# Optimization experiments

Measured on AMD Instinct MI355X. Metric: run time of the kernel, lower is better.

Reference implementation:

```python
import jax, jax.numpy as jnp
import numpy as np

LAM = 0.43
IN_DIM = 256
BATCH = 512


def _persistence_pairs(D):
    """0-dim persistence pairs via Kruskal-style union-find (matches torch code).
    D: [n, n] numpy distance matrix. Returns [n-1, 2] int array of MST edges."""
    n = D.shape[0]
    parent = np.arange(n)

    def find(u):
        root = u
        while parent[root] != root:
            root = parent[root]
        while parent[u] != root:  # path compression
            parent[u], u = root, parent[u]
        return root

    iu, ju = np.triu_indices(n)  # includes diagonal, like triu_indices_from
    w = D[iu, ju]
    order = np.argsort(w, kind='stable')
    pairs = []
    for e in order:
        u, v = int(iu[e]), int(ju[e])
        ru, rv = find(u), find(v)
        if ru == rv:
            continue
        if ru > rv:
            parent[rv] = ru  # merge(v, u)
        else:
            parent[ru] = rv  # merge(u, v)
        pairs.append((u, v) if u < v else (v, u))
    return np.asarray(pairs, dtype=np.int64)  # exactly n-1 edges


def _pdist(x):
    # torch.norm(x[:, None] - x, dim=2, p=2)
    return jnp.linalg.norm(x[:, None, :] - x[None, :, :], axis=-1)


def setup_inputs() -> dict:
    key = jax.random.key(0)
    ks = jax.random.split(key, 16)
    d = IN_DIM
    dims = [(d, d // 2), (d // 2, d // 4), (d // 4, 2), (2, d // 4), (d // 4, d // 2), (d // 2, d)]
    inp = {
        'x': jax.random.normal(ks[0], (BATCH, d), dtype=jnp.float32),
        'label': jax.random.randint(ks[1], (BATCH,), 0, 10),
    }
    names = ['1', '2', 'm', '3', '4', '5']
    for i, (nm, (din, dout)) in enumerate(zip(names, dims)):
        s = 1.0 / np.sqrt(din)
        inp['W' + nm] = jax.random.uniform(ks[2 + 2 * i], (din, dout), minval=-s, maxval=s, dtype=jnp.float32)
        inp['b' + nm] = jax.random.uniform(ks[3 + 2 * i], (dout,), minval=-s, maxval=s, dtype=jnp.float32)
    inp['latent_norm'] = jnp.ones((1,), dtype=jnp.float32)
    return inp


def reference(x, label, W1, b1, W2, b2, Wm, bm, W3, b3, W4, b4, W5, b5, latent_norm):
    # Encoder
    h1 = jax.nn.relu(x @ W1 + b1)
    h2 = jax.nn.relu(h1 @ W2 + b2)
    lat = h2 @ Wm + bm  # [B, 2]

    # normalized pairwise distance matrices
    xd = _pdist(x)
    xd = xd / xd.max()  # 2D-input branch
    ld = _pdist(lat) / latent_norm[0]

    # Decoder
    h3 = jax.nn.relu(lat @ W3 + b3)
    h4 = jax.nn.relu(h3 @ W4 + b4)
    xr = h4 @ W5 + b5
    ae_loss = jnp.mean((x - xr) ** 2)

    # persistence pairs (detached / host computation, as in the torch code)
    p1 = _persistence_pairs(np.asarray(jax.device_get(xd)))
    p2 = _persistence_pairs(np.asarray(jax.device_get(ld)))

    sig1 = xd[p1[:, 0], p1[:, 1]]
    sig1_2 = ld[p1[:, 0], p1[:, 1]]
    sig2 = ld[p2[:, 0], p2[:, 1]]
    sig2_1 = xd[p2[:, 0], p2[:, 1]]
    topo = jnp.sum((sig1 - sig1_2) ** 2) + jnp.sum((sig2 - sig2_1) ** 2)

    loss = ae_loss + LAM * topo / float(x.shape[0])
    return loss
```

## Files before the change

### kernel.cpp

```cpp
#include <hip/hip_runtime.h>
#include <math.h>

#define N      512
#define DIN    256
#define LAM    0.43f
#define MAGIC  0x4D535431u
#define PAD(j) ((j) + (((j) >> 6) << 2))

#define OFF_LDREADY 4
#define OFF_T0READY 5
#define OFF_T0BITS  6
#define OFF_BLKMAX  8
#define OFF_AEPART  128
#define OFF_LAT     1024
#define OFF_XD      2048
#define OFF_LD      (2048 + 262144)
#define OFF_CAND    526336
#define OFF_BAR     (OFF_CAND + 18432)

__device__ __forceinline__ unsigned ld_acq(unsigned* p) {
    return __hip_atomic_load(p, __ATOMIC_ACQUIRE, __HIP_MEMORY_SCOPE_AGENT);
}
__device__ __forceinline__ void st_rel(unsigned* p, unsigned v) {
    __hip_atomic_store(p, v, __ATOMIC_RELEASE, __HIP_MEMORY_SCOPE_AGENT);
}
__device__ __forceinline__ unsigned ld_rlx(unsigned* p) {
    return __hip_atomic_load(p, __ATOMIC_RELAXED, __HIP_MEMORY_SCOPE_AGENT);
}
__device__ __forceinline__ unsigned long long ld64_rlx(unsigned long long* p) {
    return __hip_atomic_load(p, __ATOMIC_RELAXED, __HIP_MEMORY_SCOPE_AGENT);
}
__device__ __forceinline__ void st64_rlx(unsigned long long* p, unsigned long long v) {
    __hip_atomic_store(p, v, __ATOMIC_RELAXED, __HIP_MEMORY_SCOPE_AGENT);
}
__device__ __forceinline__ void spin_magic(unsigned* p) {
    while (ld_acq(p) != MAGIC) __builtin_amdgcn_s_sleep(1);
}

__global__ __launch_bounds__(256) void fused_mlp_pdistx_kernel(
    const float* __restrict__ x,
    const float* __restrict__ W1, const float* __restrict__ b1,
    const float* __restrict__ W2, const float* __restrict__ b2,
    const float* __restrict__ Wm, const float* __restrict__ bm,
    const float* __restrict__ W3, const float* __restrict__ b3,
    const float* __restrict__ W4, const float* __restrict__ b4,
    const float* __restrict__ W5, const float* __restrict__ b5,
    float* __restrict__ lat_out, float* __restrict__ ae_part,
    float* __restrict__ xd, float* __restrict__ blkmax)
{
    const int tid = threadIdx.x;

    if (blockIdx.x < 512) {
        __shared__ float xs[256];
        __shared__ float h1[128];
        __shared__ float h2[64];
        __shared__ float latv[2];
        __shared__ float h3[64];
        __shared__ float h4[128];
        __shared__ float red[4];

        const int row = blockIdx.x;
        xs[tid] = x[(size_t)row * DIN + tid];
        __syncthreads();

        if (tid < 128) {
            float s = b1[tid];
            for (int k = 0; k < 256; ++k) s = fmaf(xs[k], W1[k * 128 + tid], s);
            h1[tid] = fmaxf(s, 0.f);
        }
        __syncthreads();

        if (tid < 64) {
            float s = b2[tid];
            for (int k = 0; k < 128; ++k) s = fmaf(h1[k], W2[k * 64 + tid], s);
            h2[tid] = fmaxf(s, 0.f);
        }
        __syncthreads();

        if (tid < 2) {
            float s = bm[tid];
            for (int k = 0; k < 64; ++k) s = fmaf(h2[k], Wm[k * 2 + tid], s);
            latv[tid] = s;
            lat_out[(size_t)row * 2 + tid] = s;
        }
        __syncthreads();

        if (tid < 64) {
            float s = b3[tid];
            s = fmaf(latv[0], W3[tid], s);
            s = fmaf(latv[1], W3[64 + tid], s);
            h3[tid] = fmaxf(s, 0.f);
        }
        __syncthreads();

        if (tid < 128) {
            float s = b4[tid];
            for (int k = 0; k < 64; ++k) s = fmaf(h3[k], W4[k * 128 + tid], s);
            h4[tid] = fmaxf(s, 0.f);
        }
        __syncthreads();

        float s = b5[tid];
        for (int k = 0; k < 128; ++k) s = fmaf(h4[k], W5[k * 256 + tid], s);
        float diff = xs[tid] - s;
        float a = diff * diff;

        #pragma unroll
        for (int m = 1; m < 64; m <<= 1) a += __shfl_xor(a, m, 64);
        if ((tid & 63) == 0) red[tid >> 6] = a;
        __syncthreads();
        if (tid == 0) ae_part[row] = red[0] + red[1] + red[2] + red[3];
    } else {
        __shared__ float As[32][65];
        __shared__ float Bs[32][65];
        __shared__ float red2[4];

        const int bid = blockIdx.x - 512;
        const int bi = bid & 7, bj = bid >> 3;
        const int i0 = bi * 64, j0 = bj * 64;
        const int ty = tid >> 4, tx = tid & 15;

        float acc[4][4];
        #pragma unroll
        for (int i = 0; i < 4; ++i)
            #pragma unroll
            for (int j = 0; j < 4; ++j) acc[i][j] = 0.f;

        for (int kk = 0; kk < DIN; kk += 32) {
            #pragma unroll
            for (int s = tid; s < 512; s += 256) {
                int r = s >> 3, c4 = (s & 7) << 2;
                float4 va = *(const float4*)(x + (size_t)(i0 + r) * DIN + kk + c4);
                As[c4 + 0][r] = va.x; As[c4 + 1][r] = va.y;
                As[c4 + 2][r] = va.z; As[c4 + 3][r] = va.w;
                float4 vb = *(const float4*)(x + (size_t)(j0 + r) * DIN + kk + c4);
                Bs[c4 + 0][r] = vb.x; Bs[c4 + 1][r] = vb.y;
                Bs[c4 + 2][r] = vb.z; Bs[c4 + 3][r] = vb.w;
            }
            __syncthreads();
            #pragma unroll 8
            for (int k = 0; k < 32; ++k) {
                float a[4], b[4];
                #pragma unroll
                for (int i = 0; i < 4; ++i) a[i] = As[k][ty + 16 * i];
                #pragma unroll
                for (int j = 0; j < 4; ++j) b[j] = Bs[k][tx + 16 * j];
                #pragma unroll
                for (int i = 0; i < 4; ++i)
                    #pragma unroll
                    for (int j = 0; j < 4; ++j) {
                        float d = a[i] - b[j];
                        acc[i][j] = fmaf(d, d, acc[i][j]);
                    }
            }
            __syncthreads();
        }

        float lmax = 0.f;
        #pragma unroll
        for (int i = 0; i < 4; ++i)
            #pragma unroll
            for (int j = 0; j < 4; ++j) {
                float dd = sqrtf(acc[i][j]);
                int r = i0 + ty + 16 * i, c = j0 + tx + 16 * j;
                xd[(size_t)r * N + c] = dd;
                lmax = fmaxf(lmax, dd);
            }

        #pragma unroll
        for (int m = 32; m >= 1; m >>= 1) lmax = fmaxf(lmax, __shfl_xor(lmax, m, 64));
        if ((tid & 63) == 0) red2[tid >> 6] = lmax;
        __syncthreads();
        if (tid == 0)
            blkmax[bid] = fmaxf(fmaxf(red2[0], red2[1]), fmaxf(red2[2], red2[3]));
    }
}

__global__ __launch_bounds__(256) void mst_boruvka_kernel(
    const float* __restrict__ xd, float* __restrict__ ld,
    const float* __restrict__ lat, const float* __restrict__ latent_norm,
    const float* __restrict__ blkmax, const float* __restrict__ ae_part,
    float* __restrict__ wsf, float* __restrict__ out)
{
    __shared__ unsigned comp_a[512];
    __shared__ __align__(16) unsigned comp_s[544];
    __shared__ unsigned long long cval[512];
    __shared__ int tgt[512];
    __shared__ unsigned short eu[512], ev[512];
    __shared__ float ew[512];
    __shared__ float latx[512], laty[512];
    __shared__ float s_red[4];
    __shared__ float s_xdm;
    __shared__ int s_ecnt;

    const int tid = threadIdx.x;
    const int blk = blockIdx.x;
    const int m   = blk >> 6;
    const int wb  = blk & 63;
    const bool leader = (wb == 0);

    unsigned* ldready = (unsigned*)(wsf + OFF_LDREADY);
    unsigned* t0ready = (unsigned*)(wsf + OFF_T0READY);
    unsigned* t0bits  = (unsigned*)(wsf + OFF_T0BITS);
    unsigned long long* candm =
        (unsigned long long*)(wsf + OFF_CAND) + (size_t)m * 9 * 512;
    unsigned* bar = (unsigned*)(wsf + OFF_BAR) + (size_t)m * 640;

    const float* Dm = m ? ld : xd;
    const float* Om = m ? xd : ld;

    if (m == 1) {
        for (int i = tid; i < 512; i += 256) {
            latx[i] = lat[2 * i + 0];
            laty[i] = lat[2 * i + 1];
        }
        __syncthreads();
        const int r0 = wb << 3;
        for (int q = tid; q < 1024; q += 256) {
            int rr = r0 + (q >> 7);
            int j  = (q & 127) << 2;
            float xi = latx[rr], yi = laty[rr];
            float dx0 = xi - latx[j + 0], dy0 = yi - laty[j + 0];
            float dx1 = xi - latx[j + 1], dy1 = yi - laty[j + 1];
            float dx2 = xi - latx[j + 2], dy2 = yi - laty[j + 2];
            float dx3 = xi - latx[j + 3], dy3 = yi - laty[j + 3];
            float4 o;
            o.x = sqrtf(fmaf(dx0, dx0, dy0 * dy0));
            o.y = sqrtf(fmaf(dx1, dx1, dy1 * dy1));
            o.z = sqrtf(fmaf(dx2, dx2, dy2 * dy2));
            o.w = sqrtf(fmaf(dx3, dx3, dy3 * dy3));
            *(float4*)(ld + (size_t)rr * N + j) = o;
        }
    }

    for (int i = tid; i < 72; i += 256)
        st64_rlx(&candm[(size_t)wb * 72 + i], ~0ULL);

    for (int i = tid; i < 512; i += 256) {
        comp_a[i] = (unsigned)i;
        comp_s[PAD(i)] = (unsigned)i;
    }
    if (tid == 0) s_ecnt = 0;

    __syncthreads();
    if (tid == 0) st_rel(&bar[wb], MAGIC);
    if (tid < 64) spin_magic(&bar[tid]);
    __syncthreads();
    if (m == 1 && leader && tid == 0) st_rel(ldready, MAGIC);

    int nc = 512;
    for (int p = 0; p < 9 && nc > 1; ++p) {
        unsigned long long* cand = candm + (size_t)p * 512;

        {
            const int r  = (wb << 3) + (tid >> 5);
            const int c0 = (tid & 31) << 4;
            const unsigned cv = comp_s[PAD(r)];
            const float4* rp = (const float4*)(Dm + (size_t)r * N + c0);
            unsigned long long bk = ~0ULL;
            #pragma unroll
            for (int c = 0; c < 4; ++c) {
                float4 f = rp[c];
                int jb = c0 + 4 * c;
                int4 cc = *(const int4*)&comp_s[PAD(jb)];
                unsigned long long k;
                k = ((unsigned long long)__float_as_uint(f.x) << 18)
                  | ((unsigned long long)r << 9) | (unsigned)(jb + 0);
                if ((unsigned)cc.x != cv && k < bk) bk = k;
                k = ((unsigned long long)__float_as_uint(f.y) << 18)
                  | ((unsigned long long)r << 9) | (unsigned)(jb + 1);
                if ((unsigned)cc.y != cv && k < bk) bk = k;
                k = ((unsigned long long)__float_as_uint(f.z) << 18)
                  | ((unsigned long long)r << 9) | (unsigned)(jb + 2);
                if ((unsigned)cc.z != cv && k < bk) bk = k;
                k = ((unsigned long long)__float_as_uint(f.w) << 18)
                  | ((unsigned long long)r << 9) | (unsigned)(jb + 3);
                if ((unsigned)cc.w != cv && k < bk) bk = k;
            }
            #pragma unroll
            for (int mm = 1; mm <= 16; mm <<= 1) {
                unsigned long long o = __shfl_xor(bk, mm, 64);
                if (o < bk) bk = o;
            }
            if ((tid & 31) == 0 && bk != ~0ULL)
                atomicMin(&cand[cv], bk);
        }

        __syncthreads();
        if (tid == 0) st_rel(&bar[(p + 1) * 64 + wb], MAGIC);
        if (tid < 64) spin_magic(&bar[(p + 1) * 64 + tid]);
        __syncthreads();

        for (int i = tid; i < 512; i += 256) cval[i] = ld64_rlx(&cand[i]);
        __syncthreads();
        for (int i = tid; i < 512; i += 256) {
            int t = -1;
            if (comp_a[i] == (unsigned)i && cval[i] != ~0ULL)
                t = (int)comp_a[cval[i] & 511];
            tgt[i] = t;
        }
        __syncthreads();
        for (int i = tid; i < 512; i += 256) {
            int s = tgt[i];
            if (s >= 0 && !(tgt[s] == i && i > s)) {
                comp_a[i] = (unsigned)s;
                int e = atomicAdd(&s_ecnt, 1);
                unsigned long long c = cval[i];
                eu[e] = (unsigned short)((c >> 9) & 511);
                ev[e] = (unsigned short)(c & 511);
                ew[e] = __uint_as_float((unsigned)(c >> 18));
            }
        }
        __syncthreads();
        for (int dd = 0; dd < 9; ++dd) {
            unsigned a = comp_a[comp_a[tid]];
            unsigned b = comp_a[comp_a[tid + 256]];
            __syncthreads();
            comp_a[tid] = a; comp_a[tid + 256] = b;
            __syncthreads();
        }
        for (int i = tid; i < 512; i += 256) comp_s[PAD(i)] = comp_a[i];
        nc = 512 - s_ecnt;
        __syncthreads();
    }

    if (!leader) return;

    if (tid < 64) {
        float mx = blkmax[tid];
        #pragma unroll
        for (int mm = 32; mm >= 1; mm >>= 1)
            mx = fmaxf(mx, __shfl_xor(mx, mm, 64));
        if (tid == 0) s_xdm = mx;
    }
    __syncthreads();
    const float xdm = s_xdm;
    const float lnv = latent_norm[0];
    const float sD = (m == 0) ? 1.f / xdm : 1.f / lnv;
    const float sO = (m == 0) ? 1.f / lnv : 1.f / xdm;

    if (m == 0) {
        if (tid == 0) spin_magic(ldready);
        __syncthreads();
    }

    const int ne = s_ecnt;
    float acc = 0.f;
    for (int i = tid; i < ne; i += 256) {
        float de = ew[i];
        float oe = Om[(size_t)eu[i] * N + ev[i]];
        float c = sD * de - sO * oe;
        acc = fmaf(c, c, acc);
    }
    #pragma unroll
    for (int mm = 32; mm >= 1; mm >>= 1) acc += __shfl_xor(acc, mm, 64);
    if ((tid & 63) == 0) s_red[tid >> 6] = acc;
    __syncthreads();

    if (m == 0) {
        if (tid == 0) {
            float t0 = s_red[0] + s_red[1] + s_red[2] + s_red[3];
            __hip_atomic_store(t0bits, __float_as_uint(t0), __ATOMIC_RELAXED,
                               __HIP_MEMORY_SCOPE_AGENT);
            st_rel(t0ready, MAGIC);
        }
    } else {
        float t1 = 0.f;
        if (tid == 0) t1 = s_red[0] + s_red[1] + s_red[2] + s_red[3];
        __syncthreads();
        float a = ae_part[tid] + ae_part[tid + 256];
        #pragma unroll
        for (int mm = 32; mm >= 1; mm >>= 1) a += __shfl_xor(a, mm, 64);
        if ((tid & 63) == 0) s_red[tid >> 6] = a;
        __syncthreads();
        if (tid == 0) {
            float ae = s_red[0] + s_red[1] + s_red[2] + s_red[3];
            spin_magic(t0ready);
            float t0 = __uint_as_float(ld_rlx(t0bits));
            out[0] = ae * (1.f / (float)(N * DIN))
                   + (LAM * (t0 + t1)) * (1.f / (float)N);
        }
    }
}

extern "C" void kernel_launch(void* const* d_in, const int* in_sizes, int n_in,
                              void* d_out, int out_size, void* d_ws, size_t ws_size,
                              hipStream_t stream) {
    const float* x   = (const float*)d_in[0];
    const float* W1  = (const float*)d_in[2];
    const float* b1  = (const float*)d_in[3];
    const float* W2  = (const float*)d_in[4];
    const float* b2  = (const float*)d_in[5];
    const float* Wm  = (const float*)d_in[6];
    const float* bm  = (const float*)d_in[7];
    const float* W3  = (const float*)d_in[8];
    const float* b3  = (const float*)d_in[9];
    const float* W4  = (const float*)d_in[10];
    const float* b4  = (const float*)d_in[11];
    const float* W5  = (const float*)d_in[12];
    const float* b5  = (const float*)d_in[13];
    const float* latent_norm = (const float*)d_in[14];

    float* ws      = (float*)d_ws;
    float* blkmax  = ws + OFF_BLKMAX;
    float* ae_part = ws + OFF_AEPART;
    float* lat     = ws + OFF_LAT;
    float* xd      = ws + OFF_XD;
    float* ld      = ws + OFF_LD;

    fused_mlp_pdistx_kernel<<<576, 256, 0, stream>>>(
        x, W1, b1, W2, b2, Wm, bm, W3, b3, W4, b4, W5, b5,
        lat, ae_part, xd, blkmax);
    mst_boruvka_kernel<<<128, 256, 0, stream>>>(
        xd, ld, lat, latent_norm, blkmax, ae_part, ws, (float*)d_out);
}
```

Baseline: 159.2 us.

## Replace cross-block Boruvka rounds with per-row top-16 lists and single-block MST

Each of the 64 blocks per matrix now extracts the 16 smallest packed edge keys per row and writes them to workspace, then signals once. Only the leader block continues, running all Boruvka phases locally in LDS from the top-16 lists, with a per-row cursor and a fallback full-row rescan when a row's list is exhausted. This removes the per-phase grid-wide spin barriers and global atomics. In exchange the top-k extraction adds 16 wave-wide reduction passes per row, and the MST phases are serialized onto one block per matrix.

```diff
diff --git a/kernel.cpp b/kernel.cpp
--- a/kernel.cpp
+++ b/kernel.cpp
@@ -1,11 +1,12 @@
 #include <hip/hip_runtime.h>
 #include <math.h>
+
+typedef unsigned long long ull;
 
 #define N      512
 #define DIN    256
 #define LAM    0.43f
 #define MAGIC  0x4D535431u
-#define PAD(j) ((j) + (((j) >> 6) << 2))
 
 #define OFF_LDREADY 4
 #define OFF_T0READY 5
@@ -15,8 +16,8 @@
 #define OFF_LAT     1024
 #define OFF_XD      2048
 #define OFF_LD      (2048 + 262144)
-#define OFF_CAND    526336
-#define OFF_BAR     (OFF_CAND + 18432)
+#define OFF_TOP     526336
+#define OFF_BAR     (OFF_TOP + 32768)
 
 __device__ __forceinline__ unsigned ld_acq(unsigned* p) {
     return __hip_atomic_load(p, __ATOMIC_ACQUIRE, __HIP_MEMORY_SCOPE_AGENT);
@@ -26,12 +27,6 @@
 }
 __device__ __forceinline__ unsigned ld_rlx(unsigned* p) {
     return __hip_atomic_load(p, __ATOMIC_RELAXED, __HIP_MEMORY_SCOPE_AGENT);
-}
-__device__ __forceinline__ unsigned long long ld64_rlx(unsigned long long* p) {
-    return __hip_atomic_load(p, __ATOMIC_RELAXED, __HIP_MEMORY_SCOPE_AGENT);
-}
-__device__ __forceinline__ void st64_rlx(unsigned long long* p, unsigned long long v) {
-    __hip_atomic_store(p, v, __ATOMIC_RELAXED, __HIP_MEMORY_SCOPE_AGENT);
 }
 __device__ __forceinline__ void spin_magic(unsigned* p) {
     while (ld_acq(p) != MAGIC) __builtin_amdgcn_s_sleep(1);
@@ -176,46 +171,47 @@
     }
 }
 
-__global__ __launch_bounds__(256) void mst_boruvka_kernel(
+__global__ __launch_bounds__(256) void mst_topk_kernel(
     const float* __restrict__ xd, float* __restrict__ ld,
     const float* __restrict__ lat, const float* __restrict__ latent_norm,
     const float* __restrict__ blkmax, const float* __restrict__ ae_part,
     float* __restrict__ wsf, float* __restrict__ out)
 {
+    __shared__ ull tl[8192];
     __shared__ unsigned comp_a[512];
-    __shared__ __align__(16) unsigned comp_s[544];
-    __shared__ unsigned long long cval[512];
+    __shared__ ull cand[512];
     __shared__ int tgt[512];
+    __shared__ int cur[512];
+    __shared__ int fbq[512];
     __shared__ unsigned short eu[512], ev[512];
     __shared__ float ew[512];
     __shared__ float latx[512], laty[512];
     __shared__ float s_red[4];
     __shared__ float s_xdm;
-    __shared__ int s_ecnt;
+    __shared__ int s_ecnt, s_nq;
 
     const int tid = threadIdx.x;
     const int blk = blockIdx.x;
     const int m   = blk >> 6;
     const int wb  = blk & 63;
-    const bool leader = (wb == 0);
+    const int wave = tid >> 6, lane = tid & 63;
+    const int r0 = wb << 3;
 
     unsigned* ldready = (unsigned*)(wsf + OFF_LDREADY);
     unsigned* t0ready = (unsigned*)(wsf + OFF_T0READY);
     unsigned* t0bits  = (unsigned*)(wsf + OFF_T0BITS);
-    unsigned long long* candm =
-        (unsigned long long*)(wsf + OFF_CAND) + (size_t)m * 9 * 512;
-    unsigned* bar = (unsigned*)(wsf + OFF_BAR) + (size_t)m * 640;
+    ull* top = (ull*)(wsf + OFF_TOP) + (size_t)m * 8192;
+    unsigned* bar = (unsigned*)(wsf + OFF_BAR) + (size_t)m * 64;
 
     const float* Dm = m ? ld : xd;
     const float* Om = m ? xd : ld;
 
     if (m == 1) {
         for (int i = tid; i < 512; i += 256) {
-            latx[i] = lat[2 * i + 0];
-            laty[i] = lat[2 * i + 1];
-        }
-        __syncthreads();
-        const int r0 = wb << 3;
+            float2 v = *(const float2*)(lat + 2 * i);
+            latx[i] = v.x; laty[i] = v.y;
+        }
+        __syncthreads();
         for (int q = tid; q < 1024; q += 256) {
             int rr = r0 + (q >> 7);
             int j  = (q & 127) << 2;
@@ -231,72 +227,101 @@
             o.w = sqrtf(fmaf(dx3, dx3, dy3 * dy3));
             *(float4*)(ld + (size_t)rr * N + j) = o;
         }
-    }
-
-    for (int i = tid; i < 72; i += 256)
-        st64_rlx(&candm[(size_t)wb * 72 + i], ~0ULL);
-
-    for (int i = tid; i < 512; i += 256) {
-        comp_a[i] = (unsigned)i;
-        comp_s[PAD(i)] = (unsigned)i;
-    }
-    if (tid == 0) s_ecnt = 0;
-
+        __syncthreads();
+    }
+
+    #pragma unroll
+    for (int rr = 0; rr < 2; ++rr) {
+        const int r = r0 + (wave << 1) + rr;
+        const float4* rp = (const float4*)(Dm + (size_t)r * N + (lane << 3));
+        float4 fa = rp[0], fb = rp[1];
+        float wv[8] = {fa.x, fa.y, fa.z, fa.w, fb.x, fb.y, fb.z, fb.w};
+        ull k[8];
+        #pragma unroll
+        for (int s = 0; s < 8; ++s) {
+            int j = (lane << 3) + s;
+            k[s] = (j == r) ? ~0ULL
+                 : (((ull)__float_as_uint(wv[s]) << 18) | ((ull)r << 9) | (unsigned)j);
+        }
+        for (int e = 0; e < 16; ++e) {
+            ull bk = k[0];
+            #pragma unroll
+            for (int s = 1; s < 8; ++s) bk = (k[s] < bk) ? k[s] : bk;
+            #pragma unroll
+            for (int mm = 1; mm <= 32; mm <<= 1) {
+                ull o = __shfl_xor(bk, mm, 64);
+                if (o < bk) bk = o;
+            }
+            #pragma unroll
+            for (int s = 0; s < 8; ++s) if (k[s] == bk) k[s] = ~0ULL;
+            if (lane == 0) top[(size_t)r * 16 + e] = bk;
+        }
+    }
     __syncthreads();
     if (tid == 0) st_rel(&bar[wb], MAGIC);
+    if (wb != 0) return;
+
     if (tid < 64) spin_magic(&bar[tid]);
     __syncthreads();
-    if (m == 1 && leader && tid == 0) st_rel(ldready, MAGIC);
+    if (m == 1 && tid == 0) st_rel(ldready, MAGIC);
+
+    for (int i = tid; i < 8192; i += 256) tl[i] = top[i];
+    for (int i = tid; i < 512; i += 256) { comp_a[i] = (unsigned)i; cur[i] = 0; }
+    if (tid == 0) s_ecnt = 0;
+    __syncthreads();
 
     int nc = 512;
-    for (int p = 0; p < 9 && nc > 1; ++p) {
-        unsigned long long* cand = candm + (size_t)p * 512;
-
-        {
-            const int r  = (wb << 3) + (tid >> 5);
-            const int c0 = (tid & 31) << 4;
-            const unsigned cv = comp_s[PAD(r)];
-            const float4* rp = (const float4*)(Dm + (size_t)r * N + c0);
-            unsigned long long bk = ~0ULL;
-            #pragma unroll
-            for (int c = 0; c < 4; ++c) {
-                float4 f = rp[c];
-                int jb = c0 + 4 * c;
-                int4 cc = *(const int4*)&comp_s[PAD(jb)];
-                unsigned long long k;
-                k = ((unsigned long long)__float_as_uint(f.x) << 18)
-                  | ((unsigned long long)r << 9) | (unsigned)(jb + 0);
-                if ((unsigned)cc.x != cv && k < bk) bk = k;
-                k = ((unsigned long long)__float_as_uint(f.y) << 18)
-                  | ((unsigned long long)r << 9) | (unsigned)(jb + 1);
-                if ((unsigned)cc.y != cv && k < bk) bk = k;
-                k = ((unsigned long long)__float_as_uint(f.z) << 18)
-                  | ((unsigned long long)r << 9) | (unsigned)(jb + 2);
-                if ((unsigned)cc.z != cv && k < bk) bk = k;
-                k = ((unsigned long long)__float_as_uint(f.w) << 18)
-                  | ((unsigned long long)r << 9) | (unsigned)(jb + 3);
-                if ((unsigned)cc.w != cv && k < bk) bk = k;
-            }
-            #pragma unroll
-            for (int mm = 1; mm <= 16; mm <<= 1) {
-                unsigned long long o = __shfl_xor(bk, mm, 64);
+    for (int ph = 0; ph < 9 && nc > 1; ++ph) {
+        for (int i = tid; i < 512; i += 256) cand[i] = ~0ULL;
+        if (tid == 0) s_nq = 0;
+        __syncthreads();
+
+        #pragma unroll
+        for (int rr = 0; rr < 2; ++rr) {
+            int r = tid + (rr << 8);
+            unsigned c = comp_a[r];
+            int e = cur[r];
+            ull found = ~0ULL;
+            while (e < 16) {
+                ull kk = tl[r * 16 + e];
+                if (comp_a[kk & 511] != c) { found = kk; break; }
+                ++e;
+            }
+            cur[r] = e;
+            if (e == 16) { int q = atomicAdd(&s_nq, 1); fbq[q] = r; }
+            else if (found < cand[c]) atomicMin(&cand[c], found);
+        }
+        __syncthreads();
+
+        for (int q = wave; q < s_nq; q += 4) {
+            int r = fbq[q];
+            unsigned c = comp_a[r];
+            const float4* rp = (const float4*)(Dm + (size_t)r * N + (lane << 3));
+            float4 fa = rp[0], fb = rp[1];
+            float wv[8] = {fa.x, fa.y, fa.z, fa.w, fb.x, fb.y, fb.z, fb.w};
+            ull bk = ~0ULL;
+            #pragma unroll
+            for (int s = 0; s < 8; ++s) {
+                int j = (lane << 3) + s;
+                if (j != r && comp_a[j] != c) {
+                    ull kk = ((ull)__float_as_uint(wv[s]) << 18)
+                           | ((ull)r << 9) | (unsigned)j;
+                    if (kk < bk) bk = kk;
+                }
+            }
+            #pragma unroll
+            for (int mm = 1; mm <= 32; mm <<= 1) {
+                ull o = __shfl_xor(bk, mm, 64);
                 if (o < bk) bk = o;
             }
-            if ((tid & 31) == 0 && bk != ~0ULL)
-                atomicMin(&cand[cv], bk);
-        }
-
-        __syncthreads();
-        if (tid == 0) st_rel(&bar[(p + 1) * 64 + wb], MAGIC);
-        if (tid < 64) spin_magic(&bar[(p + 1) * 64 + tid]);
-        __syncthreads();
-
-        for (int i = tid; i < 512; i += 256) cval[i] = ld64_rlx(&cand[i]);
-        __syncthreads();
+            if (lane == 0 && bk != ~0ULL && bk < cand[c]) atomicMin(&cand[c], bk);
+        }
+        __syncthreads();
+
         for (int i = tid; i < 512; i += 256) {
             int t = -1;
-            if (comp_a[i] == (unsigned)i && cval[i] != ~0ULL)
-                t = (int)comp_a[cval[i] & 511];
+            if (comp_a[i] == (unsigned)i && cand[i] != ~0ULL)
+                t = (int)comp_a[cand[i] & 511];
             tgt[i] = t;
         }
         __syncthreads();
@@ -304,11 +329,11 @@
             int s = tgt[i];
             if (s >= 0 && !(tgt[s] == i && i > s)) {
                 comp_a[i] = (unsigned)s;
-                int e = atomicAdd(&s_ecnt, 1);
-                unsigned long long c = cval[i];
-                eu[e] = (unsigned short)((c >> 9) & 511);
-                ev[e] = (unsigned short)(c & 511);
-                ew[e] = __uint_as_float((unsigned)(c >> 18));
+                int e2 = atomicAdd(&s_ecnt, 1);
+                ull cc = cand[i];
+                eu[e2] = (unsigned short)((cc >> 9) & 511);
+                ev[e2] = (unsigned short)(cc & 511);
+                ew[e2] = __uint_as_float((unsigned)(cc >> 18));
             }
         }
         __syncthreads();
@@ -319,18 +344,14 @@
             comp_a[tid] = a; comp_a[tid + 256] = b;
             __syncthreads();
         }
-        for (int i = tid; i < 512; i += 256) comp_s[PAD(i)] = comp_a[i];
         nc = 512 - s_ecnt;
         __syncthreads();
     }
-
-    if (!leader) return;
 
     if (tid < 64) {
         float mx = blkmax[tid];
         #pragma unroll
-        for (int mm = 32; mm >= 1; mm >>= 1)
-            mx = fmaxf(mx, __shfl_xor(mx, mm, 64));
+        for (int mm = 32; mm >= 1; mm >>= 1) mx = fmaxf(mx, __shfl_xor(mx, mm, 64));
         if (tid == 0) s_xdm = mx;
     }
     __syncthreads();
@@ -386,6 +407,7 @@
 extern "C" void kernel_launch(void* const* d_in, const int* in_sizes, int n_in,
                               void* d_out, int out_size, void* d_ws, size_t ws_size,
                               hipStream_t stream) {
+    (void)in_sizes; (void)n_in; (void)out_size; (void)ws_size;
     const float* x   = (const float*)d_in[0];
     const float* W1  = (const float*)d_in[2];
     const float* b1  = (const float*)d_in[3];
@@ -411,6 +433,6 @@
     fused_mlp_pdistx_kernel<<<576, 256, 0, stream>>>(
         x, W1, b1, W2, b2, Wm, bm, W3, b3, W4, b4, W5, b5,
         lat, ae_part, xd, blkmax);
-    mst_boruvka_kernel<<<128, 256, 0, stream>>>(
+    mst_topk_kernel<<<128, 256, 0, stream>>>(
         xd, ld, lat, latent_norm, blkmax, ae_part, ws, (float*)d_out);
 }
```

Measured after the change: 319.6 us. +100.7%, slower.

## Keep distance rows in registers and reduce per-row Boruvka minima locally

Applied to the files above, without the earlier changes.

Each thread now keeps its 16 distance values in registers for the whole run instead of re-reading the matrix from global memory on every Boruvka pass. Each pass publishes per-row minima to a double-buffered global array, and every block folds them into per-component candidates with shared-memory atomics, replacing global 64-bit atomicMin and the per-pass candidate reset. The initial grid barrier is removed, ldready is signalled after the first pass barrier, and pointer jumping exits early once components stop changing. This trades global atomics and repeated global reads for more registers and a redundant 512-entry reduction in every block.

```diff
diff --git a/kernel.cpp b/kernel.cpp
--- a/kernel.cpp
+++ b/kernel.cpp
@@ -1,5 +1,7 @@
 #include <hip/hip_runtime.h>
 #include <math.h>
+
+typedef unsigned long long ull;
 
 #define N      512
 #define DIN    256
@@ -15,8 +17,8 @@
 #define OFF_LAT     1024
 #define OFF_XD      2048
 #define OFF_LD      (2048 + 262144)
-#define OFF_CAND    526336
-#define OFF_BAR     (OFF_CAND + 18432)
+#define OFF_ROWM    526336
+#define OFF_BAR     (OFF_ROWM + 4096)
 
 __device__ __forceinline__ unsigned ld_acq(unsigned* p) {
     return __hip_atomic_load(p, __ATOMIC_ACQUIRE, __HIP_MEMORY_SCOPE_AGENT);
@@ -27,10 +29,10 @@
 __device__ __forceinline__ unsigned ld_rlx(unsigned* p) {
     return __hip_atomic_load(p, __ATOMIC_RELAXED, __HIP_MEMORY_SCOPE_AGENT);
 }
-__device__ __forceinline__ unsigned long long ld64_rlx(unsigned long long* p) {
+__device__ __forceinline__ ull ld64_rlx(ull* p) {
     return __hip_atomic_load(p, __ATOMIC_RELAXED, __HIP_MEMORY_SCOPE_AGENT);
 }
-__device__ __forceinline__ void st64_rlx(unsigned long long* p, unsigned long long v) {
+__device__ __forceinline__ void st64_rlx(ull* p, ull v) {
     __hip_atomic_store(p, v, __ATOMIC_RELAXED, __HIP_MEMORY_SCOPE_AGENT);
 }
 __device__ __forceinline__ void spin_magic(unsigned* p) {
@@ -176,7 +178,7 @@
     }
 }
 
-__global__ __launch_bounds__(256) void mst_boruvka_kernel(
+__global__ __launch_bounds__(256) void mst_regs_kernel(
     const float* __restrict__ xd, float* __restrict__ ld,
     const float* __restrict__ lat, const float* __restrict__ latent_norm,
     const float* __restrict__ blkmax, const float* __restrict__ ae_part,
@@ -184,140 +186,136 @@
 {
     __shared__ unsigned comp_a[512];
     __shared__ __align__(16) unsigned comp_s[544];
-    __shared__ unsigned long long cval[512];
+    __shared__ ull cnd[512];
     __shared__ int tgt[512];
     __shared__ unsigned short eu[512], ev[512];
     __shared__ float ew[512];
     __shared__ float latx[512], laty[512];
     __shared__ float s_red[4];
     __shared__ float s_xdm;
-    __shared__ int s_ecnt;
+    __shared__ int s_ecnt, s_chg;
 
     const int tid = threadIdx.x;
     const int blk = blockIdx.x;
     const int m   = blk >> 6;
     const int wb  = blk & 63;
     const bool leader = (wb == 0);
+    const int r  = (wb << 3) + (tid >> 5);
+    const int c0 = (tid & 31) << 4;
 
     unsigned* ldready = (unsigned*)(wsf + OFF_LDREADY);
     unsigned* t0ready = (unsigned*)(wsf + OFF_T0READY);
     unsigned* t0bits  = (unsigned*)(wsf + OFF_T0BITS);
-    unsigned long long* candm =
-        (unsigned long long*)(wsf + OFF_CAND) + (size_t)m * 9 * 512;
-    unsigned* bar = (unsigned*)(wsf + OFF_BAR) + (size_t)m * 640;
-
-    const float* Dm = m ? ld : xd;
+    ull* rowm = (ull*)(wsf + OFF_ROWM) + (size_t)m * 1024;
+    unsigned* bar = (unsigned*)(wsf + OFF_BAR) + (size_t)m * 576;
+
     const float* Om = m ? xd : ld;
+
+    unsigned wbits[16];
 
     if (m == 1) {
         for (int i = tid; i < 512; i += 256) {
-            latx[i] = lat[2 * i + 0];
-            laty[i] = lat[2 * i + 1];
-        }
-        __syncthreads();
-        const int r0 = wb << 3;
-        for (int q = tid; q < 1024; q += 256) {
-            int rr = r0 + (q >> 7);
-            int j  = (q & 127) << 2;
-            float xi = latx[rr], yi = laty[rr];
-            float dx0 = xi - latx[j + 0], dy0 = yi - laty[j + 0];
-            float dx1 = xi - latx[j + 1], dy1 = yi - laty[j + 1];
-            float dx2 = xi - latx[j + 2], dy2 = yi - laty[j + 2];
-            float dx3 = xi - latx[j + 3], dy3 = yi - laty[j + 3];
-            float4 o;
-            o.x = sqrtf(fmaf(dx0, dx0, dy0 * dy0));
-            o.y = sqrtf(fmaf(dx1, dx1, dy1 * dy1));
-            o.z = sqrtf(fmaf(dx2, dx2, dy2 * dy2));
-            o.w = sqrtf(fmaf(dx3, dx3, dy3 * dy3));
-            *(float4*)(ld + (size_t)rr * N + j) = o;
-        }
-    }
-
-    for (int i = tid; i < 72; i += 256)
-        st64_rlx(&candm[(size_t)wb * 72 + i], ~0ULL);
+            float2 v = *(const float2*)(lat + 2 * i);
+            latx[i] = v.x; laty[i] = v.y;
+        }
+        __syncthreads();
+        const float xi = latx[r], yi = laty[r];
+        float dv[16];
+        #pragma unroll
+        for (int s = 0; s < 16; ++s) {
+            float dx = xi - latx[c0 + s], dy = yi - laty[c0 + s];
+            dv[s] = sqrtf(fmaf(dx, dx, dy * dy));
+            wbits[s] = __float_as_uint(dv[s]);
+        }
+        #pragma unroll
+        for (int q = 0; q < 4; ++q) {
+            float4 o = make_float4(dv[4 * q], dv[4 * q + 1], dv[4 * q + 2], dv[4 * q + 3]);
+            *(float4*)(ld + (size_t)r * N + c0 + 4 * q) = o;
+        }
+    } else {
+        #pragma unroll
+        for (int q = 0; q < 4; ++q) {
+            float4 f = *(const float4*)(xd + (size_t)r * N + c0 + 4 * q);
+            wbits[4 * q + 0] = __float_as_uint(f.x);
+            wbits[4 * q + 1] = __float_as_uint(f.y);
+            wbits[4 * q + 2] = __float_as_uint(f.z);
+            wbits[4 * q + 3] = __float_as_uint(f.w);
+        }
+    }
 
     for (int i = tid; i < 512; i += 256) {
         comp_a[i] = (unsigned)i;
         comp_s[PAD(i)] = (unsigned)i;
     }
     if (tid == 0) s_ecnt = 0;
-
     __syncthreads();
-    if (tid == 0) st_rel(&bar[wb], MAGIC);
-    if (tid < 64) spin_magic(&bar[tid]);
-    __syncthreads();
-    if (m == 1 && leader && tid == 0) st_rel(ldready, MAGIC);
 
     int nc = 512;
     for (int p = 0; p < 9 && nc > 1; ++p) {
-        unsigned long long* cand = candm + (size_t)p * 512;
-
-        {
-            const int r  = (wb << 3) + (tid >> 5);
-            const int c0 = (tid & 31) << 4;
-            const unsigned cv = comp_s[PAD(r)];
-            const float4* rp = (const float4*)(Dm + (size_t)r * N + c0);
-            unsigned long long bk = ~0ULL;
-            #pragma unroll
-            for (int c = 0; c < 4; ++c) {
-                float4 f = rp[c];
-                int jb = c0 + 4 * c;
-                int4 cc = *(const int4*)&comp_s[PAD(jb)];
-                unsigned long long k;
-                k = ((unsigned long long)__float_as_uint(f.x) << 18)
-                  | ((unsigned long long)r << 9) | (unsigned)(jb + 0);
-                if ((unsigned)cc.x != cv && k < bk) bk = k;
-                k = ((unsigned long long)__float_as_uint(f.y) << 18)
-                  | ((unsigned long long)r << 9) | (unsigned)(jb + 1);
-                if ((unsigned)cc.y != cv && k < bk) bk = k;
-                k = ((unsigned long long)__float_as_uint(f.z) << 18)
-                  | ((unsigned long long)r << 9) | (unsigned)(jb + 2);
-                if ((unsigned)cc.z != cv && k < bk) bk = k;
-                k = ((unsigned long long)__float_as_uint(f.w) << 18)
-                  | ((unsigned long long)r << 9) | (unsigned)(jb + 3);
-                if ((unsigned)cc.w != cv && k < bk) bk = k;
+        for (int i = tid; i < 512; i += 256) cnd[i] = ~0ULL;
+
+        const unsigned cv = comp_s[PAD(r)];
+        ull bk = ~0ULL;
+        #pragma unroll
+        for (int s = 0; s < 16; ++s) {
+            int j = c0 + s;
+            unsigned cj = comp_s[PAD(j)];
+            ull k = ((ull)wbits[s] << 18) | ((ull)r << 9) | (unsigned)j;
+            if (cj != cv && k < bk) bk = k;
+        }
+        #pragma unroll
+        for (int mm = 1; mm <= 16; mm <<= 1) {
+            ull o = __shfl_xor(bk, mm, 64);
+            if (o < bk) bk = o;
+        }
+        if ((tid & 31) == 0) st64_rlx(&rowm[(size_t)(p & 1) * 512 + r], bk);
+
+        __syncthreads();
+        if (tid == 0) st_rel(&bar[p * 64 + wb], MAGIC);
+        if (tid < 64) spin_magic(&bar[p * 64 + tid]);
+        __syncthreads();
+        if (p == 0 && m == 1 && leader && tid == 0)
+            st_rel(ldready, MAGIC);
+
+        for (int i = tid; i < 512; i += 256) {
+            ull kk = ld64_rlx(&rowm[(size_t)(p & 1) * 512 + i]);
+            if (kk != ~0ULL) {
+                unsigned c = comp_a[i];
+                if (kk < cnd[c]) atomicMin(&cnd[c], kk);
             }
-            #pragma unroll
-            for (int mm = 1; mm <= 16; mm <<= 1) {
-                unsigned long long o = __shfl_xor(bk, mm, 64);
-                if (o < bk) bk = o;
-            }
-            if ((tid & 31) == 0 && bk != ~0ULL)
-                atomicMin(&cand[cv], bk);
-        }
-
-        __syncthreads();
-        if (tid == 0) st_rel(&bar[(p + 1) * 64 + wb], MAGIC);
-        if (tid < 64) spin_magic(&bar[(p + 1) * 64 + tid]);
-        __syncthreads();
-
-        for (int i = tid; i < 512; i += 256) cval[i] = ld64_rlx(&cand[i]);
-        __syncthreads();
+        }
+        __syncthreads();
+
         for (int i = tid; i < 512; i += 256) {
             int t = -1;
-            if (comp_a[i] == (unsigned)i && cval[i] != ~0ULL)
-                t = (int)comp_a[cval[i] & 511];
+            if (comp_a[i] == (unsigned)i && cnd[i] != ~0ULL)
+                t = (int)comp_a[cnd[i] & 511];
             tgt[i] = t;
         }
         __syncthreads();
         for (int i = tid; i < 512; i += 256) {
-            int s = tgt[i];
-            if (s >= 0 && !(tgt[s] == i && i > s)) {
-                comp_a[i] = (unsigned)s;
+            int s2 = tgt[i];
+            if (s2 >= 0 && !(tgt[s2] == i && i > s2)) {
+                comp_a[i] = (unsigned)s2;
                 int e = atomicAdd(&s_ecnt, 1);
-                unsigned long long c = cval[i];
-                eu[e] = (unsigned short)((c >> 9) & 511);
-                ev[e] = (unsigned short)(c & 511);
-                ew[e] = __uint_as_float((unsigned)(c >> 18));
+                ull cc = cnd[i];
+                eu[e] = (unsigned short)((cc >> 9) & 511);
+                ev[e] = (unsigned short)(cc & 511);
+                ew[e] = __uint_as_float((unsigned)(cc >> 18));
             }
         }
         __syncthreads();
+
         for (int dd = 0; dd < 9; ++dd) {
+            if (tid == 0) s_chg = 0;
+            __syncthreads();
             unsigned a = comp_a[comp_a[tid]];
             unsigned b = comp_a[comp_a[tid + 256]];
+            if (a != comp_a[tid] || b != comp_a[tid + 256]) s_chg = 1;
             __syncthreads();
             comp_a[tid] = a; comp_a[tid + 256] = b;
             __syncthreads();
+            if (!s_chg) break;
         }
         for (int i = tid; i < 512; i += 256) comp_s[PAD(i)] = comp_a[i];
         nc = 512 - s_ecnt;
@@ -329,8 +327,7 @@
     if (tid < 64) {
         float mx = blkmax[tid];
         #pragma unroll
-        for (int mm = 32; mm >= 1; mm >>= 1)
-            mx = fmaxf(mx, __shfl_xor(mx, mm, 64));
+        for (int mm = 32; mm >= 1; mm >>= 1) mx = fmaxf(mx, __shfl_xor(mx, mm, 64));
         if (tid == 0) s_xdm = mx;
     }
     __syncthreads();
@@ -386,6 +383,7 @@
 extern "C" void kernel_launch(void* const* d_in, const int* in_sizes, int n_in,
                               void* d_out, int out_size, void* d_ws, size_t ws_size,
                               hipStream_t stream) {
+    (void)in_sizes; (void)n_in; (void)out_size; (void)ws_size;
     const float* x   = (const float*)d_in[0];
     const float* W1  = (const float*)d_in[2];
     const float* b1  = (const float*)d_in[3];
@@ -411,6 +409,6 @@
     fused_mlp_pdistx_kernel<<<576, 256, 0, stream>>>(
         x, W1, b1, W2, b2, Wm, bm, W3, b3, W4, b4, W5, b5,
         lat, ae_part, xd, blkmax);
-    mst_boruvka_kernel<<<128, 256, 0, stream>>>(
+    mst_regs_kernel<<<128, 256, 0, stream>>>(
         xd, ld, lat, latent_norm, blkmax, ae_part, ws, (float*)d_out);
 }
```

Result: faster. 151.4 us (-4.9%).
